# Kernel optimization log

Measured on AMD Instinct MI355X. Metric: run time of the kernel, lower is better.

## Reference

```python
import jax, jax.numpy as jnp
from jax import lax
import numpy as np

V, EMB, ELMO, WORD, H, B, R, L = 11322, 300, 1024, 512, 512, 32, 10, 20


def setup_inputs():
    key = jax.random.key(0)
    ks = jax.random.split(key, 24)

    def n(k, shape, s=0.02):
        return jax.random.normal(k, shape, dtype=jnp.float32) * s

    inp = {}
    inp["ques"] = jax.random.randint(ks[0], (B, R, L), 0, V)
    inp["hist"] = jax.random.randint(ks[1], (B, R, 2 * L), 0, V)
    inp["ques_len"] = jax.random.randint(ks[2], (B, R), 1, L + 1)
    inp["hist_len"] = jax.random.randint(ks[3], (B, R), 1, 2 * L + 1)
    inp["img_feat"] = n(ks[4], (B, 36, 2048), 1.0)
    inp["v_relations"] = n(ks[5], (B, 36, 36, 512), 1.0)
    inp["w_emb"] = n(ks[6], (V, EMB))          # GloVe/numberbatch table
    inp["elmo_emb"] = n(ks[7], (V, ELMO))      # frozen ELMo table
    inp["Wc"] = n(ks[8], (WORD, ELMO))         # embed_change Linear
    inp["bc"] = jnp.zeros((WORD,), jnp.float32)
    IN0 = EMB + WORD                            # LSTM layer-0 input size = 812
    names = ["q_Wih0", "q_Whh0", "q_b0", "q_Wih1", "q_Whh1", "q_b1",
             "h_Wih0", "h_Whh0", "h_b0", "h_Wih1", "h_Whh1", "h_b1"]
    shapes = [(4 * H, IN0), (4 * H, H), (4 * H,), (4 * H, H), (4 * H, H), (4 * H,)] * 2
    for i, (nm, sh) in enumerate(zip(names, shapes)):
        inp[nm] = n(ks[9 + i], sh, 0.04)
    return inp


def lstm_layer(x, Wih, Whh, b):
    # x: [N, T, In] -> all hidden states [N, T, H]; PyTorch gate order i,f,g,o
    N = x.shape[0]
    Hh = Whh.shape[1]
    xproj = jnp.einsum('nti,gi->ntg', x, Wih) + b  # [N, T, 4H]

    def step(carry, xp):
        h, c = carry
        gates = xp + h @ Whh.T
        i, f, g, o = jnp.split(gates, 4, axis=-1)
        c = jax.nn.sigmoid(f) * c + jax.nn.sigmoid(i) * jnp.tanh(g)
        h = jax.nn.sigmoid(o) * jnp.tanh(c)
        return (h, c), h

    h0 = jnp.zeros((N, Hh), x.dtype)
    _, hs = lax.scan(step, (h0, h0), jnp.swapaxes(xproj, 0, 1))
    return jnp.swapaxes(hs, 0, 1)


def encode(tokens, lens, w_emb, elmo_emb, Wc, bc, Wih0, Whh0, b0, Wih1, Whh1, b1):
    # Embedding lookup + elmo->word projection, 2-layer LSTM, take h at t = len-1
    Ntok = tokens.shape[0]
    emb = w_emb[tokens]                         # [N, T, 300]
    elmo = elmo_emb[tokens] @ Wc.T + bc         # [N, T, 512] (dropout off: eval)
    x = jnp.concatenate([emb, elmo], axis=-1)   # [N, T, 812]
    h1 = lstm_layer(x, Wih0, Whh0, b0)
    h2 = lstm_layer(h1, Wih1, Whh1, b1)
    return h2[jnp.arange(Ntok), lens - 1]       # DynamicRNN: last valid hidden


def reference(ques, hist, ques_len, hist_len, img_feat, v_relations, w_emb, elmo_emb, Wc, bc,
              q_Wih0, q_Whh0, q_b0, q_Wih1, q_Whh1, q_b1,
              h_Wih0, h_Whh0, h_b0, h_Wih1, h_Whh1, h_b1):
    Bq, Rr, Ll = ques.shape
    ques_embed = encode(ques.reshape(Bq * Rr, Ll), ques_len.reshape(-1),
                        w_emb, elmo_emb, Wc, bc,
                        q_Wih0, q_Whh0, q_b0, q_Wih1, q_Whh1, q_b1).reshape(Bq, Rr, -1)
    hist_embed = encode(hist.reshape(Bq * Rr, 2 * Ll), hist_len.reshape(-1),
                        w_emb, elmo_emb, Wc, bc,
                        h_Wih0, h_Whh0, h_b0, h_Wih1, h_Whh1, h_b1).reshape(Bq, Rr, -1)
    # Vectorized form of the Python double loop + pad_sequence:
    # f_history[b, i, j] = hist_embed[b, j] if j <= i else 0   -> [B, R, R, H]
    tri = jnp.tril(jnp.ones((Rr, Rr), hist_embed.dtype))
    f_history = hist_embed[:, None, :, :] * tri[None, :, :, None]
    # masks exactly as t_rel.abs().sum(-1).bool() on the broadcast tensors
    m = (jnp.abs(f_history).sum(-1) != 0)       # [B, R, R]
    # t_rel[b,i,j,k,:] = f_history[b,i,j,:] zeroed where tmp (=f_history[b,i,k]) is zero
    t_rel = f_history[:, :, :, None, :] * m[:, :, None, :, None]
    tmp = f_history[:, :, None, :, :] * m[:, :, :, None, None]
    text_rel = jnp.concatenate([t_rel, tmp], axis=-1)  # [B, R, R, R, 2H]
    return ques_embed, text_rel
```

## Files before the change

kernel.cpp:

```cpp
#include <hip/hip_runtime.h>
#include <math.h>

#define NSEQ 320
#define HDIM 512
#define G4   2048
#define EMBD 300
#define ELMOD 1024
#define XPAD 832
#define BUFU (160*1024)

typedef __attribute__((ext_vector_type(8))) short bf16x8;
typedef __attribute__((ext_vector_type(4))) float f32x4;
typedef __attribute__((ext_vector_type(4))) unsigned int u32x4;
typedef __attribute__((ext_vector_type(2))) unsigned int u32x2;
typedef unsigned short ushort_t;

__device__ __forceinline__ float sigmoidf_(float x) { return 1.0f / (1.0f + expf(-x)); }

__device__ __forceinline__ ushort_t f2bf(float f) {
    unsigned u = __float_as_uint(f);
    u = (u + 0x7FFFu + ((u >> 16) & 1u)) >> 16;
    return (ushort_t)u;
}
__device__ __forceinline__ unsigned pack2(float a, float b) {
    return (unsigned)f2bf(a) | ((unsigned)f2bf(b) << 16);
}

struct ConvPack {
    const float* src[9];
    ushort_t* dst[9];
    int srcCols[9], dstStride[9], dstOff[9], fillCols[9];
    long base[10];
};

__global__ __launch_bounds__(256) void conv_all_kernel(ConvPack P)
{
    long gid = (long)blockIdx.x * 256 + threadIdx.x;
    if (gid >= P.base[9]) return;
    int job = 0;
    #pragma unroll
    for (int j = 1; j < 9; ++j) if (gid >= P.base[j]) job = j;
    int e  = (int)(gid - P.base[job]);
    int fc = P.fillCols[job];
    int r  = e / fc;
    int ci = e - r * fc;
    int sc = P.srcCols[job];
    float v = (ci < sc) ? P.src[job][(size_t)r * sc + ci] : 0.0f;
    P.dst[job][(size_t)r * P.dstStride[job] + P.dstOff[job] + ci] = f2bf(v);
}

__global__ __launch_bounds__(128) void emb_gather_kernel(
    const int* __restrict__ ques, const int* __restrict__ hist,
    const float* __restrict__ w_emb, ushort_t* __restrict__ Xb)
{
    int n = blockIdx.x;
    int tokid = (n < 6400) ? ques[n] : hist[n - 6400];
    int t = threadIdx.x;
    ushort_t* dst = Xb + (size_t)n * XPAD;
    if (t < 75) {
        const float4* src = (const float4*)(w_emb + (size_t)tokid * EMBD);
        float4 v = src[t];
        dst[4*t+0] = f2bf(v.x); dst[4*t+1] = f2bf(v.y);
        dst[4*t+2] = f2bf(v.z); dst[4*t+3] = f2bf(v.w);
    } else if (t >= 108) {
        dst[812 + (t - 108)] = 0;
    }
}

__global__ __launch_bounds__(256) void gemm_ff_kernel(
    const ushort_t* __restrict__ Ab, const float* __restrict__ Af,
    const int* __restrict__ tok, int strideA,
    const ushort_t* __restrict__ W, const float* __restrict__ bias,
    ushort_t* __restrict__ C, int strideC, int K, int remap)
{
    __shared__ ushort_t As[64 * 40];
    __shared__ ushort_t Bs[64 * 40];
    const int m0 = blockIdx.y * 64;
    const int n0 = blockIdx.x * 64;
    const int tid = threadIdx.x;
    const int r  = tid >> 2;
    const int kq = (tid & 3) << 3;

    const ushort_t* arow_b = nullptr;
    const float*    arow_f = nullptr;
    if (Af) arow_f = Af + (size_t)tok[m0 + r] * strideA + kq;
    else    arow_b = Ab + (size_t)(m0 + r) * strideA + kq;
    const ushort_t* brow = W + (size_t)(n0 + r) * K + kq;

    const int lane = tid & 63;
    const int w = tid >> 6;
    const int wm = w & 1, wn = w >> 1;
    const int kc = (lane >> 4) << 3;

    f32x4 acc[2][2];
    #pragma unroll
    for (int f = 0; f < 2; ++f)
        #pragma unroll
        for (int g = 0; g < 2; ++g)
            acc[f][g] = (f32x4){0.f, 0.f, 0.f, 0.f};

    for (int k0 = 0; k0 < K; k0 += 32) {
        if (Af) {
            float4 v0 = ((const float4*)(arow_f + k0))[0];
            float4 v1 = ((const float4*)(arow_f + k0))[1];
            uint4 p; p.x = pack2(v0.x, v0.y); p.y = pack2(v0.z, v0.w);
            p.z = pack2(v1.x, v1.y); p.w = pack2(v1.z, v1.w);
            *(uint4*)&As[r*40 + kq] = p;
        } else {
            *(uint4*)&As[r*40 + kq] = *(const uint4*)(arow_b + k0);
        }
        *(uint4*)&Bs[r*40 + kq] = *(const uint4*)(brow + k0);
        __syncthreads();
        bf16x8 af[2], bfr[2];
        #pragma unroll
        for (int f = 0; f < 2; ++f)
            af[f] = *(const bf16x8*)&As[(wm*32 + f*16 + (lane & 15))*40 + kc];
        #pragma unroll
        for (int g = 0; g < 2; ++g)
            bfr[g] = *(const bf16x8*)&Bs[(wn*32 + g*16 + (lane & 15))*40 + kc];
        #pragma unroll
        for (int f = 0; f < 2; ++f)
            #pragma unroll
            for (int g = 0; g < 2; ++g)
                acc[f][g] = __builtin_amdgcn_mfma_f32_16x16x32_bf16(af[f], bfr[g], acc[f][g], 0, 0, 0);
        __syncthreads();
    }

    #pragma unroll
    for (int f = 0; f < 2; ++f) {
        #pragma unroll
        for (int g = 0; g < 2; ++g) {
            int col = n0 + wn*32 + g*16 + (lane & 15);
            float bv = bias[col];
            int colw = remap ? ((col & 511) * 4 + (col >> 9)) : col;
            #pragma unroll
            for (int i = 0; i < 4; ++i) {
                int row = m0 + wm*32 + f*16 + ((lane >> 4) << 2) + i;
                C[(size_t)row * strideC + colw] = f2bf(acc[f][g][i] + bv);
            }
        }
    }
}

struct PCellN {
    ushort_t* rot;
    const ushort_t* B;
    const ushort_t* xp;
    const float* bias;
    float* hlast;
    const int* lens;
    int* lctr;
    int* pflag;
    int K, T, layer;
};
struct PPackN { PCellN cell[8]; };

template<int N> __device__ __forceinline__ void vmwait() {
    if constexpr      (N == 0)  asm volatile("s_waitcnt vmcnt(0)"  ::: "memory");
    else if constexpr (N == 1)  asm volatile("s_waitcnt vmcnt(1)"  ::: "memory");
    else if constexpr (N == 2)  asm volatile("s_waitcnt vmcnt(2)"  ::: "memory");
    else if constexpr (N == 3)  asm volatile("s_waitcnt vmcnt(3)"  ::: "memory");
    else if constexpr (N == 4)  asm volatile("s_waitcnt vmcnt(4)"  ::: "memory");
    else if constexpr (N == 5)  asm volatile("s_waitcnt vmcnt(5)"  ::: "memory");
    else if constexpr (N == 6)  asm volatile("s_waitcnt vmcnt(6)"  ::: "memory");
    else if constexpr (N == 7)  asm volatile("s_waitcnt vmcnt(7)"  ::: "memory");
    else if constexpr (N == 8)  asm volatile("s_waitcnt vmcnt(8)"  ::: "memory");
    else if constexpr (N == 9)  asm volatile("s_waitcnt vmcnt(9)"  ::: "memory");
    else if constexpr (N == 10) asm volatile("s_waitcnt vmcnt(10)" ::: "memory");
    else if constexpr (N == 11) asm volatile("s_waitcnt vmcnt(11)" ::: "memory");
    else if constexpr (N == 12) asm volatile("s_waitcnt vmcnt(12)" ::: "memory");
    else if constexpr (N == 13) asm volatile("s_waitcnt vmcnt(13)" ::: "memory");
    else if constexpr (N == 14) asm volatile("s_waitcnt vmcnt(14)" ::: "memory");
    else                        asm volatile("s_waitcnt vmcnt(15)" ::: "memory");
}

template<int C, int NQ, int D>
__device__ __forceinline__ void aissN(uint4 (&ap)[D][NQ],
    const ushort_t* baseX, const ushort_t* baseH, const int* aoff)
{
    const ushort_t* b_ = (C * 32 < 512) ? baseX : baseH;
    #pragma unroll
    for (int q = 0; q < NQ; ++q)
        asm volatile("global_load_dwordx4 %0, %1, off"
            : "=v"(ap[C % D][q])
            : "v"((const char*)b_ + aoff[q] + C * 64));
}

template<int C, int D, int NQ>
__device__ __forceinline__ void prologueN(uint4 (&ap)[D][NQ],
    const ushort_t* bX, const ushort_t* bH, const int* aoff)
{
    if constexpr (C < D) {
        aissN<C, NQ, D>(ap, bX, bH, aoff);
        prologueN<C + 1, D, NQ>(ap, bX, bH, aoff);
    }
}

template<int C, int NC, int NQ, int D>
__device__ __forceinline__ void chunksN(uint4 (&ap)[D][NQ], f32x4 (&acc)[NQ][4],
    const ushort_t* bX, const ushort_t* bH, const int* aoff,
    const ushort_t* Bs, int PK, int cc, int kg)
{
    if constexpr (C < NC) {
        constexpr int infl = (NC - 1 - C) > (D - 1) ? (D - 1) : (NC - 1 - C);
        vmwait<infl * NQ>();
        __builtin_amdgcn_sched_barrier(0);
        bf16x8 bfr[4];
        #pragma unroll
        for (int g = 0; g < 4; ++g)
            bfr[g] = *(const bf16x8*)&Bs[(g*16 + cc)*PK + C*32 + kg*8];
        #pragma unroll
        for (int q = 0; q < NQ; ++q)
            #pragma unroll
            for (int g = 0; g < 4; ++g)
                acc[q][g] = __builtin_amdgcn_mfma_f32_16x16x32_bf16(
                    *(const bf16x8*)&ap[C % D][q], bfr[g], acc[q][g], 0, 0, 0);
        if constexpr (C + D < NC) aissN<C + D, NQ, D>(ap, bX, bH, aoff);
        chunksN<C + 1, NC, NQ, D>(ap, acc, bX, bH, aoff, Bs, PK, cc, kg);
    }
}

template<int NC, int NQ, int D>
__device__ __forceinline__ void step_work(
    const ushort_t* __restrict__ baseX,
    const ushort_t* __restrict__ baseH,
    const ushort_t* __restrict__ Bs, int PK,
    const ushort_t* __restrict__ xp,
    const float* __restrict__ bias_r,
    ushort_t* __restrict__ Ost,
    float* __restrict__ hlast,
    const unsigned* __restrict__ lr,
    float (&creg)[3][4],
    int t, int T, int tq0, int lane, int j)
{
    const int cc = lane & 15, kg = lane >> 4;

    int aoff[NQ];
    #pragma unroll
    for (int q = 0; q < NQ; ++q)
        aoff[q] = ((tq0 + q)*16 + cc)*2048 + kg*16;

    u32x2 xpk[NQ][4];
    if (xp) {
        #pragma unroll
        for (int q = 0; q < NQ; ++q)
            #pragma unroll
            for (int i = 0; i < 4; ++i) {
                const int n = (tq0 + q)*16 + kg*4 + i;
                asm volatile("global_load_dwordx2 %0, %1, off"
                    : "=v"(xpk[q][i])
                    : "v"((const char*)xp + ((size_t)n*T + t)*4096 + (size_t)j*8));
            }
    }

    f32x4 acc[NQ][4];
    #pragma unroll
    for (int q = 0; q < NQ; ++q)
        #pragma unroll
        for (int g = 0; g < 4; ++g)
            acc[q][g] = (f32x4){0.f, 0.f, 0.f, 0.f};

    uint4 ap[D][NQ];
    prologueN<0, D, NQ>(ap, baseX, baseH, aoff);
    chunksN<0, NC, NQ, D>(ap, acc, baseX, baseH, aoff, Bs, PK, cc, kg);
    __builtin_amdgcn_sched_barrier(0);

    #pragma unroll
    for (int q = 0; q < NQ; ++q) {
        const unsigned lq = lr[q];
        #pragma unroll
        for (int i = 0; i < 4; ++i) {
            const int n = (tq0 + q)*16 + kg*4 + i;
            float g0 = acc[q][0][i], g1 = acc[q][1][i];
            float g2 = acc[q][2][i], g3 = acc[q][3][i];
            if (xp) {
                u32x2 xv = xpk[q][i];
                g0 += __uint_as_float(xv.x << 16);
                g1 += __uint_as_float(xv.x & 0xFFFF0000u);
                g2 += __uint_as_float(xv.y << 16);
                g3 += __uint_as_float(xv.y & 0xFFFF0000u);
            } else {
                g0 += bias_r[0]; g1 += bias_r[1];
                g2 += bias_r[2]; g3 += bias_r[3];
            }
            float cn = sigmoidf_(g1) * creg[q][i] + sigmoidf_(g0) * tanhf(g2);
            creg[q][i] = cn;
            float h = sigmoidf_(g3) * tanhf(cn);
            unsigned hb = (unsigned)f2bf(h);
            unsigned pb = (unsigned)__shfl_xor((int)hb, 1);
            if ((cc & 1) == 0) {
                ushort_t* oa = Ost + (size_t)n * 1024 + j;
                asm volatile("global_store_dword %0, %1, off sc0 sc1"
                             :: "v"(oa), "v"(hb | (pb << 16)));
            }
            if (hlast && t == (int)((lq >> (8*i)) & 0xFF) - 1)
                hlast[(size_t)n * HDIM + j] = h;
        }
    }
}

__global__ __launch_bounds__(256) void lstm_persist_kernel(PPackN P)
{
    const int inst = blockIdx.x & 7;
    const int blk  = blockIdx.x >> 3;
    const PCellN cl = P.cell[inst];

    const int tid  = threadIdx.x;
    const int w    = tid >> 6;
    const int lane = tid & 63;
    const int cc   = lane & 15;
    const int kg   = lane >> 4;
    const int j0   = blk * 16;
    const int j    = j0 + cc;
    const int K = cl.K, T = cl.T, PK = K + 8;
    const int nq  = (w < 2) ? 3 : 2;
    const int tq0 = (w < 2) ? w*3 : 6 + (w - 2)*2;

    __shared__ ushort_t Bs[64 * 1032];

    {
        const int CH = K >> 3;
        const int tot = 64 * CH;
        for (int idx = tid; idx < tot; idx += 256) {
            int r = idx / CH, ch = idx - r * CH;
            int gr = (r >> 4) * HDIM + j0 + (r & 15);
            *(u32x4*)&Bs[r * PK + ch * 8] = *(const u32x4*)(cl.B + (size_t)gr * K + ch * 8);
        }
    }

    float bias_r[4] = {0.f, 0.f, 0.f, 0.f};
    if (cl.bias) {
        #pragma unroll
        for (int g = 0; g < 4; ++g) bias_r[g] = cl.bias[g * HDIM + j];
    }

    unsigned lr[3] = {0u, 0u, 0u};
    #pragma unroll
    for (int q = 0; q < 3; ++q) {
        if (q < nq) {
            unsigned pkd = 0;
            #pragma unroll
            for (int i = 0; i < 4; ++i)
                pkd |= ((unsigned)cl.lens[(tq0 + q)*16 + kg*4 + i] & 0xFF) << (8*i);
            lr[q] = pkd;
        }
    }

    float creg[3][4];
    #pragma unroll
    for (int q = 0; q < 3; ++q)
        #pragma unroll
        for (int i = 0; i < 4; ++i) creg[q][i] = 0.f;

    __syncthreads();

    for (int ss = 0; ss <= T; ++ss) {
        const bool active = cl.layer ? (ss >= 1) : (ss < T);
        if (active) {
            const int t = cl.layer ? (ss - 1) : ss;
            const ushort_t* baseX; const ushort_t* baseH; ushort_t* Ost;
            if (cl.layer == 0) {
                baseX = cl.rot + (size_t)t * BUFU;
                baseH = baseX;
                Ost   = cl.rot + (size_t)(t + 1) * BUFU;
            } else {
                baseX = cl.rot + (size_t)(t + 1) * BUFU;
                baseH = cl.rot + (size_t)t * BUFU;
                Ost   = cl.rot + (size_t)(t + 1) * BUFU + HDIM;
            }
            if (K == 512) {
                if (w < 2) step_work<16,3,6>(baseX, baseH, Bs, PK, cl.xp, bias_r, Ost, cl.hlast, lr, creg, t, T, tq0, lane, j);
                else       step_work<16,2,8>(baseX, baseH, Bs, PK, cl.xp, bias_r, Ost, cl.hlast, lr, creg, t, T, tq0, lane, j);
            } else {
                if (w < 2) step_work<32,3,6>(baseX, baseH, Bs, PK, cl.xp, bias_r, Ost, cl.hlast, lr, creg, t, T, tq0, lane, j);
                else       step_work<32,2,8>(baseX, baseH, Bs, PK, cl.xp, bias_r, Ost, cl.hlast, lr, creg, t, T, tq0, lane, j);
            }
        }
        if (ss < T) {
            asm volatile("s_waitcnt vmcnt(0)" ::: "memory");
            __syncthreads();
            if (tid == 0) {
                __hip_atomic_fetch_add(cl.lctr, 1, __ATOMIC_RELAXED, __HIP_MEMORY_SCOPE_AGENT);
                const int tgt = 32 * (ss + 1);
                int spins = 0;
                while (__hip_atomic_load(cl.lctr, __ATOMIC_RELAXED, __HIP_MEMORY_SCOPE_AGENT) < tgt) {
                    __builtin_amdgcn_s_sleep(1);
                    if (++spins > (1 << 20)) break;
                }
                if (cl.layer == 0) {
                    if (blk == 0)
                        __hip_atomic_store(cl.pflag, ss + 1, __ATOMIC_RELAXED, __HIP_MEMORY_SCOPE_AGENT);
                } else {
                    spins = 0;
                    while (__hip_atomic_load(cl.pflag, __ATOMIC_RELAXED, __HIP_MEMORY_SCOPE_AGENT) < ss + 1) {
                        __builtin_amdgcn_s_sleep(1);
                        if (++spins > (1 << 20)) break;
                    }
                }
            }
            __syncthreads();
        }
    }
}

__global__ __launch_bounds__(64) void nz_kernel(
    const float* __restrict__ he, int* __restrict__ nz)
{
    int rr = blockIdx.x;
    int lane = threadIdx.x;
    const float* row = he + (size_t)rr * HDIM;
    bool any = false;
    for (int k = lane; k < HDIM; k += 64) any |= (row[k] != 0.0f);
    unsigned long long b = __ballot(any);
    if (lane == 0) nz[rr] = (b != 0ull) ? 1 : 0;
}

__global__ __launch_bounds__(256) void expand_kernel(
    const float* __restrict__ he, const int* __restrict__ nz,
    float* __restrict__ out)
{
    int blk = blockIdx.x;
    int k = blk % 10;
    int j = (blk / 10) % 10;
    int i = (blk / 100) % 10;
    int b = blk / 1000;
    int tid = threadIdx.x;
    float4* o = (float4*)(out + (size_t)blk * 1024);
    float4 z; z.x = z.y = z.z = z.w = 0.0f;
    if (tid < 128) {
        bool m = (j <= i) && (k <= i) && (nz[b*10 + k] != 0);
        float4 v = m ? ((const float4*)(he + (size_t)(b*10 + j) * HDIM))[tid] : z;
        o[tid] = v;
    } else {
        int c = tid - 128;
        bool m = (k <= i) && (j <= i) && (nz[b*10 + j] != 0);
        float4 v = m ? ((const float4*)(he + (size_t)(b*10 + k) * HDIM))[c] : z;
        o[128 + c] = v;
    }
}

extern "C" void kernel_launch(void* const* d_in, const int* in_sizes, int n_in,
                              void* d_out, int out_size, void* d_ws, size_t ws_size,
                              hipStream_t stream)
{
    (void)in_sizes; (void)n_in; (void)out_size; (void)ws_size;
    const int* ques     = (const int*)d_in[0];
    const int* hist     = (const int*)d_in[1];
    const int* ques_len = (const int*)d_in[2];
    const int* hist_len = (const int*)d_in[3];
    const float* w_emb  = (const float*)d_in[6];
    const float* elmo   = (const float*)d_in[7];
    const float* Wc     = (const float*)d_in[8];
    const float* bc     = (const float*)d_in[9];

    char* ws = (char*)d_ws;
    size_t off = 0;
    auto alloc = [&](size_t bytes) { char* p = ws + off; off += (bytes + 255) & ~(size_t)255; return p; };
    ushort_t* XP0bf = (ushort_t*)alloc((size_t)19200 * G4 * 2);

    const size_t rotSlice = (size_t)41 * BUFU * 2;
    char* uni = alloc(4 * rotSlice);
    ushort_t* Xb = (ushort_t*)uni;
    auto rotPtr = [&](int s, int v) { return (ushort_t*)(uni + (size_t)(s*2 + v) * rotSlice); };

    ushort_t* Wcb = (ushort_t*)alloc((size_t)HDIM * ELMOD * 2);
    ushort_t *Wih0b[2], *Whh0b[2], *Wcat[2];
    for (int s = 0; s < 2; ++s) {
        Wih0b[s] = (ushort_t*)alloc((size_t)G4 * XPAD * 2);
        Whh0b[s] = (ushort_t*)alloc((size_t)G4 * HDIM * 2);
        Wcat[s]  = (ushort_t*)alloc((size_t)G4 * ELMOD * 2);
    }
    int* ctrs = (int*)alloc(4096);
    float* he = (float*)alloc((size_t)NSEQ * HDIM * 4);
    int* nzb  = (int*)alloc(NSEQ * 4);

    float* out = (float*)d_out;
    float* ques_embed = out;
    float* text_rel   = out + (size_t)NSEQ * HDIM;

    const int rowoff[2] = {0, 6400};
    const int TT[2] = {20, 40};
    const int* lensp[2] = {ques_len, hist_len};

    ConvPack CP;
    {
        int ji = 0; long base = 0;
        auto addJob = [&](const float* src, ushort_t* dst, int sc, int ds, int doff, int fc, int rows) {
            CP.src[ji] = src; CP.dst[ji] = dst; CP.srcCols[ji] = sc; CP.dstStride[ji] = ds;
            CP.dstOff[ji] = doff; CP.fillCols[ji] = fc; CP.base[ji] = base;
            base += (long)fc * rows; ++ji;
        };
        addJob(Wc, Wcb, ELMOD, ELMOD, 0, ELMOD, HDIM);
        for (int s = 0; s < 2; ++s) {
            addJob((const float*)d_in[10 + 6*s], Wih0b[s], 812,  XPAD,  0,    XPAD, G4);
            addJob((const float*)d_in[11 + 6*s], Whh0b[s], HDIM, HDIM,  0,    HDIM, G4);
            addJob((const float*)d_in[13 + 6*s], Wcat[s],  HDIM, ELMOD, 0,    HDIM, G4);
            addJob((const float*)d_in[14 + 6*s], Wcat[s],  HDIM, ELMOD, HDIM, HDIM, G4);
        }
        CP.base[9] = base;
        int nblk = (int)((base + 255) / 256);
        conv_all_kernel<<<nblk, 256, 0, stream>>>(CP);
    }

    emb_gather_kernel<<<19200, 128, 0, stream>>>(ques, hist, w_emb, Xb);
    for (int s = 0; s < 2; ++s) {
        int Ntok = NSEQ * TT[s];
        ushort_t* XbS = Xb + (size_t)rowoff[s] * XPAD;
        const int* tok = s ? hist : ques;
        gemm_ff_kernel<<<dim3(HDIM/64, Ntok/64), 256, 0, stream>>>(
            nullptr, elmo, tok, ELMOD, Wcb, bc, XbS + EMBD, XPAD, ELMOD, 0);
        const float* b0 = (const float*)d_in[12 + 6*s];
        gemm_ff_kernel<<<dim3(G4/64, Ntok/64), 256, 0, stream>>>(
            XbS, nullptr, nullptr, XPAD, Wih0b[s], b0,
            XP0bf + (size_t)rowoff[s] * G4, G4, XPAD, 1);
    }

    hipMemsetAsync(ctrs, 0, 4096, stream);
    for (int s = 0; s < 2; ++s)
        for (int v = 0; v < 2; ++v)
            hipMemsetAsync(rotPtr(s, v), 0, (size_t)BUFU * 2, stream);

    PPackN P;
    for (int layer = 0; layer < 2; ++layer)
        for (int s = 0; s < 2; ++s)
            for (int v = 0; v < 2; ++v) {
                PCellN& c = P.cell[layer*4 + s*2 + v];
                c.rot   = rotPtr(s, v);
                c.B     = layer ? Wcat[s] : Whh0b[s];
                c.xp    = layer ? nullptr
                                : XP0bf + (size_t)(rowoff[s] + v*160*TT[s]) * G4;
                c.bias  = layer ? (const float*)d_in[15 + 6*s] : nullptr;
                c.hlast = layer ? ((s ? he : ques_embed) + (size_t)v*160*HDIM) : nullptr;
                c.lens  = lensp[s] + v*160;
                c.lctr  = ctrs + (layer*4 + s*2 + v) * 64;
                c.pflag = ctrs + 512 + (s*2 + v) * 64;
                c.K = layer ? ELMOD : HDIM;
                c.T = TT[s];
                c.layer = layer;
            }
    lstm_persist_kernel<<<256, 256, 0, stream>>>(P);

    nz_kernel<<<NSEQ, 64, 0, stream>>>(he, nzb);
    expand_kernel<<<32000, 256, 0, stream>>>(he, nzb, text_rel);
}
```

Before: 991.0 us.

## Replace atomic-counter grid barrier with per-block flags and XOR-swizzle LDS weights

The inter-block step barrier in the persistent LSTM kernel no longer uses a shared atomic counter polled by one thread. Each block now writes its step number to its own flag slot with system-coherent stores, and a full wavefront polls all 32 flags and checks them with a wave-wide all-reduce. Separately, the padded LDS layout for the recurrent weights is replaced by an unpadded layout with an XOR swizzle, which avoids bank conflicts without the padding. The aim is to cut per-step barrier latency and atomic contention, at the cost of more polling traffic and relying on the coherence behaviour of the sc0/sc1 bits.

```diff
diff --git a/kernel.cpp b/kernel.cpp
--- a/kernel.cpp
+++ b/kernel.cpp
@@ -149,7 +149,7 @@
     const float* bias;
     float* hlast;
     const int* lens;
-    int* lctr;
+    int* flags;
     int* pflag;
     int K, T, layer;
 };
@@ -199,7 +199,7 @@
 template<int C, int NC, int NQ, int D>
 __device__ __forceinline__ void chunksN(uint4 (&ap)[D][NQ], f32x4 (&acc)[NQ][4],
     const ushort_t* bX, const ushort_t* bH, const int* aoff,
-    const ushort_t* Bs, int PK, int cc, int kg)
+    const ushort_t* Bs, int cc, int kg, int swz)
 {
     if constexpr (C < NC) {
         constexpr int infl = (NC - 1 - C) > (D - 1) ? (D - 1) : (NC - 1 - C);
@@ -207,8 +207,10 @@
         __builtin_amdgcn_sched_barrier(0);
         bf16x8 bfr[4];
         #pragma unroll
-        for (int g = 0; g < 4; ++g)
-            bfr[g] = *(const bf16x8*)&Bs[(g*16 + cc)*PK + C*32 + kg*8];
+        for (int g = 0; g < 4; ++g) {
+            int boff = ((g*16 + cc) * (NC*64) + C*64 + kg*16) ^ swz;
+            bfr[g] = *(const bf16x8*)((const char*)Bs + boff);
+        }
         #pragma unroll
         for (int q = 0; q < NQ; ++q)
             #pragma unroll
@@ -216,7 +218,7 @@
                 acc[q][g] = __builtin_amdgcn_mfma_f32_16x16x32_bf16(
                     *(const bf16x8*)&ap[C % D][q], bfr[g], acc[q][g], 0, 0, 0);
         if constexpr (C + D < NC) aissN<C + D, NQ, D>(ap, bX, bH, aoff);
-        chunksN<C + 1, NC, NQ, D>(ap, acc, bX, bH, aoff, Bs, PK, cc, kg);
+        chunksN<C + 1, NC, NQ, D>(ap, acc, bX, bH, aoff, Bs, cc, kg, swz);
     }
 }
 
@@ -224,7 +226,7 @@
 __device__ __forceinline__ void step_work(
     const ushort_t* __restrict__ baseX,
     const ushort_t* __restrict__ baseH,
-    const ushort_t* __restrict__ Bs, int PK,
+    const ushort_t* __restrict__ Bs,
     const ushort_t* __restrict__ xp,
     const float* __restrict__ bias_r,
     ushort_t* __restrict__ Ost,
@@ -234,6 +236,7 @@
     int t, int T, int tq0, int lane, int j)
 {
     const int cc = lane & 15, kg = lane >> 4;
+    const int swz = (cc & 7) << 4;
 
     int aoff[NQ];
     #pragma unroll
@@ -262,7 +265,7 @@
 
     uint4 ap[D][NQ];
     prologueN<0, D, NQ>(ap, baseX, baseH, aoff);
-    chunksN<0, NC, NQ, D>(ap, acc, baseX, baseH, aoff, Bs, PK, cc, kg);
+    chunksN<0, NC, NQ, D>(ap, acc, baseX, baseH, aoff, Bs, cc, kg, swz);
     __builtin_amdgcn_sched_barrier(0);
 
     #pragma unroll
@@ -312,11 +315,11 @@
     const int kg   = lane >> 4;
     const int j0   = blk * 16;
     const int j    = j0 + cc;
-    const int K = cl.K, T = cl.T, PK = K + 8;
+    const int K = cl.K, T = cl.T;
     const int nq  = (w < 2) ? 3 : 2;
     const int tq0 = (w < 2) ? w*3 : 6 + (w - 2)*2;
 
-    __shared__ ushort_t Bs[64 * 1032];
+    __shared__ ushort_t Bs[64 * 1024];
 
     {
         const int CH = K >> 3;
@@ -324,7 +327,8 @@
         for (int idx = tid; idx < tot; idx += 256) {
             int r = idx / CH, ch = idx - r * CH;
             int gr = (r >> 4) * HDIM + j0 + (r & 15);
-            *(u32x4*)&Bs[r * PK + ch * 8] = *(const u32x4*)(cl.B + (size_t)gr * K + ch * 8);
+            int dst = (idx * 16) ^ ((r & 7) << 4);
+            *(u32x4*)((char*)Bs + dst) = *(const u32x4*)(cl.B + (size_t)gr * K + ch * 8);
         }
     }
 
@@ -369,33 +373,47 @@
                 Ost   = cl.rot + (size_t)(t + 1) * BUFU + HDIM;
             }
             if (K == 512) {
-                if (w < 2) step_work<16,3,6>(baseX, baseH, Bs, PK, cl.xp, bias_r, Ost, cl.hlast, lr, creg, t, T, tq0, lane, j);
-                else       step_work<16,2,8>(baseX, baseH, Bs, PK, cl.xp, bias_r, Ost, cl.hlast, lr, creg, t, T, tq0, lane, j);
+                if (w < 2) step_work<16,3,6>(baseX, baseH, Bs, cl.xp, bias_r, Ost, cl.hlast, lr, creg, t, T, tq0, lane, j);
+                else       step_work<16,2,8>(baseX, baseH, Bs, cl.xp, bias_r, Ost, cl.hlast, lr, creg, t, T, tq0, lane, j);
             } else {
-                if (w < 2) step_work<32,3,6>(baseX, baseH, Bs, PK, cl.xp, bias_r, Ost, cl.hlast, lr, creg, t, T, tq0, lane, j);
-                else       step_work<32,2,8>(baseX, baseH, Bs, PK, cl.xp, bias_r, Ost, cl.hlast, lr, creg, t, T, tq0, lane, j);
+                if (w < 2) step_work<32,3,6>(baseX, baseH, Bs, cl.xp, bias_r, Ost, cl.hlast, lr, creg, t, T, tq0, lane, j);
+                else       step_work<32,2,8>(baseX, baseH, Bs, cl.xp, bias_r, Ost, cl.hlast, lr, creg, t, T, tq0, lane, j);
             }
         }
         if (ss < T) {
             asm volatile("s_waitcnt vmcnt(0)" ::: "memory");
             __syncthreads();
             if (tid == 0) {
-                __hip_atomic_fetch_add(cl.lctr, 1, __ATOMIC_RELAXED, __HIP_MEMORY_SCOPE_AGENT);
-                const int tgt = 32 * (ss + 1);
-                int spins = 0;
-                while (__hip_atomic_load(cl.lctr, __ATOMIC_RELAXED, __HIP_MEMORY_SCOPE_AGENT) < tgt) {
-                    __builtin_amdgcn_s_sleep(1);
-                    if (++spins > (1 << 20)) break;
-                }
+                int* fa = cl.flags + blk;
+                int vv = ss + 1;
+                asm volatile("global_store_dword %0, %1, off sc0 sc1"
+                             :: "v"(fa), "v"(vv) : "memory");
+            }
+            if (w == 0) {
+                const int* fa = cl.flags + (lane & 31);
+                int spins = 0; bool ok;
+                do {
+                    int v;
+                    asm volatile("global_load_dword %0, %1, off sc0 sc1"
+                                 : "=v"(v) : "v"(fa) : "memory");
+                    asm volatile("s_waitcnt vmcnt(0)" ::: "memory");
+                    ok = (bool)__all(v >= ss + 1);
+                    if (!ok) __builtin_amdgcn_s_sleep(1);
+                } while (!ok && ++spins < (1 << 20));
                 if (cl.layer == 0) {
-                    if (blk == 0)
-                        __hip_atomic_store(cl.pflag, ss + 1, __ATOMIC_RELAXED, __HIP_MEMORY_SCOPE_AGENT);
-                } else {
-                    spins = 0;
-                    while (__hip_atomic_load(cl.pflag, __ATOMIC_RELAXED, __HIP_MEMORY_SCOPE_AGENT) < ss + 1) {
-                        __builtin_amdgcn_s_sleep(1);
-                        if (++spins > (1 << 20)) break;
+                    if (blk == 0 && lane == 0) {
+                        int vv = ss + 1;
+                        asm volatile("global_store_dword %0, %1, off sc0 sc1"
+                                     :: "v"(cl.pflag), "v"(vv) : "memory");
                     }
+                } else if (lane == 0) {
+                    int spins2 = 0; int pv;
+                    do {
+                        asm volatile("global_load_dword %0, %1, off sc0 sc1"
+                                     : "=v"(pv) : "v"((const int*)cl.pflag) : "memory");
+                        asm volatile("s_waitcnt vmcnt(0)" ::: "memory");
+                        if (pv < ss + 1) __builtin_amdgcn_s_sleep(1);
+                    } while (pv < ss + 1 && ++spins2 < (1 << 20));
                 }
             }
             __syncthreads();
@@ -524,7 +542,8 @@
     for (int layer = 0; layer < 2; ++layer)
         for (int s = 0; s < 2; ++s)
             for (int v = 0; v < 2; ++v) {
-                PCellN& c = P.cell[layer*4 + s*2 + v];
+                int inst = layer*4 + s*2 + v;
+                PCellN& c = P.cell[inst];
                 c.rot   = rotPtr(s, v);
                 c.B     = layer ? Wcat[s] : Whh0b[s];
                 c.xp    = layer ? nullptr
@@ -532,8 +551,8 @@
                 c.bias  = layer ? (const float*)d_in[15 + 6*s] : nullptr;
                 c.hlast = layer ? ((s ? he : ques_embed) + (size_t)v*160*HDIM) : nullptr;
                 c.lens  = lensp[s] + v*160;
-                c.lctr  = ctrs + (layer*4 + s*2 + v) * 64;
-                c.pflag = ctrs + 512 + (s*2 + v) * 64;
+                c.flags = ctrs + inst * 32;
+                c.pflag = ctrs + 512 + (s*2 + v) * 32;
                 c.K = layer ? ELMOD : HDIM;
                 c.T = TT[s];
                 c.layer = layer;
```

Measured after the change: 991.5 us. Within noise of the previous version (+0.0%).
